# Kernel tuning notes

Measured on AMD Instinct MI355X. Metric: run time of the kernel, lower is better.

## Reference

```python
import jax, jax.numpy as jnp
import numpy as np
from jax.ops import segment_sum, segment_max, segment_min

B_, T_, V_, H_, W_ = 1, 8, 6, 96, 160
NUM_TRACKS = 512          # track ids in [-1, NUM_TRACKS)
THR = 2.0                 # distance_threshold
DKS = 0.05                # duplicate_keep_scale
NEG = -1e30


def setup_inputs() -> dict:
    key = jax.random.key(0)
    ks = jax.random.split(key, 10)
    shp = (B_, T_, V_, H_, W_)
    f = lambda k, c: jax.random.normal(k, shp + (c,), jnp.float32)
    return {
        "center": f(ks[0], 3),
        "offset": f(ks[1], 3),
        "opacity": f(ks[2], 1),
        "scale": f(ks[3], 3),
        "rotation": f(ks[4], 4),
        "feat_dc": f(ks[5], 3),
        "keep_score": f(ks[6], 1),
        "instance_affinity": f(ks[7], 32),
        "motion_code": f(ks[8], 16),
        "global_track_id": jax.random.randint(ks[9], shp, -1, NUM_TRACKS),
    }


def _merge(floats, gid):
    center, offset, opacity, scale, rotation, feat_dc, keep, inst, motion = floats
    b, t, v, h, w = gid.shape
    B, N = b * t, v * h * w
    BN = B * N
    S = B * NUM_TRACKS            # one segment per (frame, track id); S = dummy segment
    nseg = S + 1

    ids = gid.reshape(BN)
    bt = jnp.arange(BN) // N
    valid = ids >= 0
    seg = jnp.where(valid, bt * NUM_TRACKS + jnp.maximum(ids, 0), S)

    # tracks with >= 2 cells participate (torch: mask.sum() < 2 -> skip)
    cnt = segment_sum(valid.astype(jnp.int32), seg, num_segments=nseg)
    dup = valid & (cnt[seg] >= 2)
    seg1 = jnp.where(dup, seg, S)

    flat = lambda x: x.reshape(BN, x.shape[-1])
    k0 = flat(keep)[:, 0]
    c = flat(center)

    def seg_softmax(mask, sgm):
        # numerically stable segment softmax of k0 restricted to mask
        m = segment_max(jnp.where(mask, k0, NEG), sgm, num_segments=nseg)
        arg = jnp.where(mask, k0 - m[sgm], 0.0)   # keep grads finite on masked lanes
        e = jnp.where(mask, jnp.exp(arg), 0.0)
        z = segment_sum(e, sgm, num_segments=nseg)
        return e / jnp.maximum(z[sgm], 1e-20), m

    # pass 1: softmax-weighted mean center over all cells of the track
    w1, _ = seg_softmax(dup, seg1)
    mc1 = segment_sum(w1[:, None] * c, seg1, num_segments=nseg)
    dist = jnp.linalg.norm(c - mc1[seg1], axis=-1)
    active = dup & (dist <= THR)

    # pass 2: softmax restricted to active cells
    seg2 = jnp.where(active, seg, S)
    w2, m2 = seg_softmax(active, seg2)

    # representative = argmax weight (== argmax keep score), first occurrence on ties
    idx = jnp.arange(BN)
    cand = jnp.where(active & (k0 == m2[seg2]), idx, BN)
    rep = segment_min(cand, seg2, num_segments=nseg)
    is_rep = active & (idx == rep[seg2])

    def wmean(x):
        xf = flat(x)
        return segment_sum(w2[:, None] * xf, seg2, num_segments=nseg)[seg2]

    mcen = wmean(center)
    moff = wmean(offset)
    mop = wmean(opacity)
    msc = wmean(scale)
    mrot_seg = segment_sum(w2[:, None] * flat(rotation), seg2, num_segments=nseg)
    mrot_seg = mrot_seg / jnp.maximum(
        jnp.linalg.norm(mrot_seg, axis=-1, keepdims=True), 1e-12)  # F.normalize
    mrot = mrot_seg[seg2]
    mfd = wmean(feat_dc)
    minst = wmean(inst)
    mmot = wmean(motion)
    kf = flat(keep)
    mkeep = segment_max(jnp.where(active[:, None], kf, NEG), seg2,
                        num_segments=nseg)[seg2]

    a = active[:, None]
    sfac = jnp.where(is_rep, 1.0, DKS)[:, None]   # duplicates suppressed
    out = jnp.concatenate([
        jnp.where(a, mcen, c),
        jnp.where(a, moff, flat(offset)),
        jnp.where(a, mop * sfac, flat(opacity)),
        jnp.where(a, msc, flat(scale)),
        jnp.where(a, mrot, flat(rotation)),
        jnp.where(a, mfd, flat(feat_dc)),
        jnp.where(a, mkeep * sfac, kf),
        jnp.where(a, minst, flat(inst)),
        jnp.where(a, mmot, flat(motion)),
    ], axis=-1)
    return out.reshape(b, t, v, h, w, -1)


def reference(center, offset, opacity, scale, rotation, feat_dc, keep_score,
              instance_affinity, motion_code, global_track_id):
    floats = (center, offset, opacity, scale, rotation, feat_dc, keep_score,
              instance_affinity, motion_code)
    return _merge(floats, global_track_id)
```

## Files before the change

### kernel.cpp

```cpp
#include <hip/hip_runtime.h>

static constexpr int kBN   = 737280;
static constexpr int kSlab = 92160;
static constexpr int kNT   = 512;
static constexpr int kNSeg = 4096;
static constexpr int kChunk = 5120;

__global__ __launch_bounds__(1024) void k_count(const int* __restrict__ gid, int* cnt) {
    __shared__ int h[kNT];
    int tid = threadIdx.x;
    if (tid < kNT) h[tid] = 0;
    __syncthreads();
    int chunk0 = blockIdx.x * kChunk;
    int bt = chunk0 / kSlab;
    for (int j = tid; j < kChunk; j += 1024) {
        int id = gid[chunk0 + j];
        if (id >= 0) atomicAdd(&h[id], 1);
    }
    __syncthreads();
    if (tid < kNT) { int v = h[tid]; if (v) atomicAdd(&cnt[bt * kNT + tid], v); }
}

__global__ __launch_bounds__(1024) void k_scan(const int* __restrict__ cnt, int* offs, int* cursor) {
    __shared__ int part[1024];
    int tid = threadIdx.x;
    int b = tid * 4;
    int v0 = cnt[b], v1 = cnt[b + 1], v2 = cnt[b + 2], v3 = cnt[b + 3];
    int s01 = v0 + v1, s = s01 + v2 + v3;
    part[tid] = s;
    __syncthreads();
    for (int off = 1; off < 1024; off <<= 1) {
        int t = (tid >= off) ? part[tid - off] : 0;
        __syncthreads();
        part[tid] += t;
        __syncthreads();
    }
    int base = part[tid] - s;
    int o0 = base, o1 = base + v0, o2 = base + s01, o3 = base + s01 + v2;
    offs[b] = o0; offs[b + 1] = o1; offs[b + 2] = o2; offs[b + 3] = o3;
    cursor[b] = o0; cursor[b + 1] = o1; cursor[b + 2] = o2; cursor[b + 3] = o3;
}

__global__ __launch_bounds__(1024) void k_fill(const int* __restrict__ gid, int* cursor, int* lists) {
    __shared__ int lcnt[kNT];
    __shared__ int lbase[kNT];
    int tid = threadIdx.x;
    if (tid < kNT) lcnt[tid] = 0;
    __syncthreads();
    int chunk0 = blockIdx.x * kChunk;
    int bt = chunk0 / kSlab;
    int rank[5], ids[5];
#pragma unroll
    for (int u = 0; u < 5; u++) {
        int id = gid[chunk0 + tid + u * 1024];
        ids[u] = id;
        rank[u] = (id >= 0) ? atomicAdd(&lcnt[id], 1) : 0;
    }
    __syncthreads();
    if (tid < kNT) { int c = lcnt[tid]; lbase[tid] = c ? atomicAdd(&cursor[bt * kNT + tid], c) : 0; }
    __syncthreads();
#pragma unroll
    for (int u = 0; u < 5; u++) {
        int id = ids[u];
        if (id >= 0) lists[lbase[id] + rank[u]] = chunk0 + tid + u * 1024;
    }
}

template<int CNT>
__device__ __forceinline__ void wreduce_store(float (&a)[17], int lane, int tb, float* totl) {
#pragma unroll
    for (int c = 0; c < CNT; c++) {
        float v = a[c];
#pragma unroll
        for (int m = 1; m < 64; m <<= 1) v += __shfl_xor(v, m, 64);
        if (lane == 0) totl[tb + c] = v;
    }
}

__global__ __launch_bounds__(256, 4) void k_seg(
        const int* __restrict__ lists, const int* __restrict__ offs, const int* __restrict__ cnt,
        const float* __restrict__ keep, const float* __restrict__ center,
        const float* __restrict__ offsetp, const float* __restrict__ opacity,
        const float* __restrict__ scale, const float* __restrict__ rot,
        const float* __restrict__ fd, const float* __restrict__ inst,
        const float* __restrict__ motion,
        float* __restrict__ out) {
    int s = ((blockIdx.x & 7) << 9) | (blockIdx.x >> 3);
    int n = cnt[s];
    if (n < 2) return;
    int base = offs[s];
    int tid = threadIdx.x;
    int lane = tid & 63;
    int wv = tid >> 6;

    __shared__ int   idxs[256];
    __shared__ float kk[256];
    __shared__ float c0s[256], c1s[256], c2s[256];
    __shared__ float e2s[256];
    __shared__ float red4[256][5];
    __shared__ float wm1[4], wm2[4];
    __shared__ int   wri[4];
    __shared__ float totl[66];
    __shared__ float mrec[66];

    float lmax = -1e30f;
    for (int j = tid; j < n; j += 256) {
        int i = lists[base + j];
        float k = keep[i];
        float cx = center[3 * i + 0], cy = center[3 * i + 1], cz = center[3 * i + 2];
        if (j < 256) { idxs[j] = i; kk[j] = k; c0s[j] = cx; c1s[j] = cy; c2s[j] = cz; }
        lmax = fmaxf(lmax, k);
    }
#pragma unroll
    for (int m = 1; m < 64; m <<= 1) lmax = fmaxf(lmax, __shfl_xor(lmax, m, 64));
    if (lane == 0) wm1[wv] = lmax;
    __syncthreads();
    float m1 = fmaxf(fmaxf(wm1[0], wm1[1]), fmaxf(wm1[2], wm1[3]));

    float lz = 0.f, l0 = 0.f, l1 = 0.f, l2 = 0.f;
    for (int j = tid; j < n; j += 256) {
        float k, cx, cy, cz;
        if (j < 256) { k = kk[j]; cx = c0s[j]; cy = c1s[j]; cz = c2s[j]; }
        else { int i = lists[base + j]; k = keep[i];
               cx = center[3 * i + 0]; cy = center[3 * i + 1]; cz = center[3 * i + 2]; }
        float e = expf(k - m1);
        lz += e; l0 += e * cx; l1 += e * cy; l2 += e * cz;
    }
    red4[tid][0] = lz; red4[tid][1] = l0; red4[tid][2] = l1; red4[tid][3] = l2;
    __syncthreads();
    for (int o = 128; o; o >>= 1) {
        if (tid < o) {
            red4[tid][0] += red4[tid + o][0]; red4[tid][1] += red4[tid + o][1];
            red4[tid][2] += red4[tid + o][2]; red4[tid][3] += red4[tid + o][3];
        }
        __syncthreads();
    }
    float z1 = red4[0][0];
    float inv1 = 1.0f / fmaxf(z1, 1e-20f);
    float mc0 = red4[0][1] * inv1, mcy = red4[0][2] * inv1, mcz = red4[0][3] * inv1;

    float lm2 = -1e30f;
    for (int j = tid; j < n; j += 256) {
        float k, cx, cy, cz;
        if (j < 256) { k = kk[j]; cx = c0s[j]; cy = c1s[j]; cz = c2s[j]; }
        else { int i = lists[base + j]; k = keep[i];
               cx = center[3 * i + 0]; cy = center[3 * i + 1]; cz = center[3 * i + 2]; }
        float d0 = cx - mc0, d1 = cy - mcy, d2 = cz - mcz;
        bool act = sqrtf(d0 * d0 + d1 * d1 + d2 * d2) <= 2.0f;
        if (j < 256) e2s[j] = act ? 1.0f : 0.0f;
        if (act) lm2 = fmaxf(lm2, k);
    }
#pragma unroll
    for (int m = 1; m < 64; m <<= 1) lm2 = fmaxf(lm2, __shfl_xor(lm2, m, 64));
    if (lane == 0) wm2[wv] = lm2;
    __syncthreads();
    float m2 = fmaxf(fmaxf(wm2[0], wm2[1]), fmaxf(wm2[2], wm2[3]));

    int lrep = 0x7fffffff;
    for (int j = tid; j < n; j += 256) {
        if (j < 256) {
            bool act = e2s[j] != 0.0f;
            float k = kk[j];
            float e = act ? expf(k - m2) : 0.0f;
            e2s[j] = e;
            if (act && k == m2) lrep = min(lrep, idxs[j]);
        } else {
            int i = lists[base + j];
            float k = keep[i];
            float cx = center[3 * i + 0], cy = center[3 * i + 1], cz = center[3 * i + 2];
            float d0 = cx - mc0, d1 = cy - mcy, d2 = cz - mcz;
            if (sqrtf(d0 * d0 + d1 * d1 + d2 * d2) <= 2.0f && k == m2) lrep = min(lrep, i);
        }
    }
#pragma unroll
    for (int m = 1; m < 64; m <<= 1) lrep = min(lrep, __shfl_xor(lrep, m, 64));
    if (lane == 0) wri[wv] = lrep;
    __syncthreads();
    int rep = min(min(wri[0], wri[1]), min(wri[2], wri[3]));

    auto e2_glob = [&](int j, int& i) -> float {
        i = lists[base + j];
        float k = keep[i];
        float d0 = center[3 * i + 0] - mc0;
        float d1 = center[3 * i + 1] - mcy;
        float d2 = center[3 * i + 2] - mcz;
        return (sqrtf(d0 * d0 + d1 * d1 + d2 * d2) <= 2.0f) ? expf(k - m2) : 0.0f;
    };

    {
        float a[17];
#pragma unroll
        for (int c = 0; c < 17; c++) a[c] = 0.f;

        if (wv == 0) {
            for (int j = lane; j < n; j += 64) {
                float e, cx, cy, cz, k; int i;
                if (j < 256) { e = e2s[j]; i = idxs[j]; cx = c0s[j]; cy = c1s[j]; cz = c2s[j]; k = kk[j]; }
                else { e = e2_glob(j, i); k = keep[i];
                       cx = center[3 * i + 0]; cy = center[3 * i + 1]; cz = center[3 * i + 2]; }
                float o0 = offsetp[3 * i + 0], o1 = offsetp[3 * i + 1], o2 = offsetp[3 * i + 2];
                float op = opacity[i];
                float s0 = scale[3 * i + 0], s1 = scale[3 * i + 1], s2 = scale[3 * i + 2];
                float4 r4 = *(const float4*)(rot + 4 * i);
                float f0 = fd[3 * i + 0], f1 = fd[3 * i + 1], f2 = fd[3 * i + 2];
                if (e != 0.0f) {
                    a[0] += e * cx; a[1] += e * cy; a[2] += e * cz;
                    a[3] += e * o0; a[4] += e * o1; a[5] += e * o2;
                    a[6] += e * op;
                    a[7] += e * s0; a[8] += e * s1; a[9] += e * s2;
                    a[10] += e * r4.x; a[11] += e * r4.y; a[12] += e * r4.z; a[13] += e * r4.w;
                    a[14] += e * f0; a[15] += e * f1; a[16] += e * f2;
                } else {
                    float* o = out + (long)66 * i;
                    o[0] = cx; o[1] = cy; o[2] = cz;
                    o[3] = o0; o[4] = o1; o[5] = o2;
                    o[6] = op;
                    o[7] = s0; o[8] = s1; o[9] = s2;
                    o[10] = r4.x; o[11] = r4.y; o[12] = r4.z; o[13] = r4.w;
                    o[14] = f0; o[15] = f1; o[16] = f2;
                    o[17] = k;
                }
            }
            wreduce_store<17>(a, lane, 0, totl);
        } else if (wv == 1) {
            for (int j = lane; j < n; j += 64) {
                float e; int i;
                if (j < 256) { e = e2s[j]; i = idxs[j]; } else { e = e2_glob(j, i); }
                const float4* ip = (const float4*)(inst + 32 * i);
                float4 v0 = ip[0], v1 = ip[1], v2 = ip[2], v3 = ip[3];
                if (e != 0.0f) {
                    a[0]  += e * v0.x; a[1]  += e * v0.y; a[2]  += e * v0.z; a[3]  += e * v0.w;
                    a[4]  += e * v1.x; a[5]  += e * v1.y; a[6]  += e * v1.z; a[7]  += e * v1.w;
                    a[8]  += e * v2.x; a[9]  += e * v2.y; a[10] += e * v2.z; a[11] += e * v2.w;
                    a[12] += e * v3.x; a[13] += e * v3.y; a[14] += e * v3.z; a[15] += e * v3.w;
                } else {
                    float2* o = (float2*)(out + (long)66 * i + 18);
                    o[0] = make_float2(v0.x, v0.y); o[1] = make_float2(v0.z, v0.w);
                    o[2] = make_float2(v1.x, v1.y); o[3] = make_float2(v1.z, v1.w);
                    o[4] = make_float2(v2.x, v2.y); o[5] = make_float2(v2.z, v2.w);
                    o[6] = make_float2(v3.x, v3.y); o[7] = make_float2(v3.z, v3.w);
                }
            }
            wreduce_store<16>(a, lane, 17, totl);
        } else if (wv == 2) {
            for (int j = lane; j < n; j += 64) {
                float e; int i;
                if (j < 256) { e = e2s[j]; i = idxs[j]; } else { e = e2_glob(j, i); }
                const float4* ip = (const float4*)(inst + 32 * i) + 4;
                float4 v0 = ip[0], v1 = ip[1], v2 = ip[2], v3 = ip[3];
                if (e != 0.0f) {
                    a[0]  += e * v0.x; a[1]  += e * v0.y; a[2]  += e * v0.z; a[3]  += e * v0.w;
                    a[4]  += e * v1.x; a[5]  += e * v1.y; a[6]  += e * v1.z; a[7]  += e * v1.w;
                    a[8]  += e * v2.x; a[9]  += e * v2.y; a[10] += e * v2.z; a[11] += e * v2.w;
                    a[12] += e * v3.x; a[13] += e * v3.y; a[14] += e * v3.z; a[15] += e * v3.w;
                } else {
                    float2* o = (float2*)(out + (long)66 * i + 34);
                    o[0] = make_float2(v0.x, v0.y); o[1] = make_float2(v0.z, v0.w);
                    o[2] = make_float2(v1.x, v1.y); o[3] = make_float2(v1.z, v1.w);
                    o[4] = make_float2(v2.x, v2.y); o[5] = make_float2(v2.z, v2.w);
                    o[6] = make_float2(v3.x, v3.y); o[7] = make_float2(v3.z, v3.w);
                }
            }
            wreduce_store<16>(a, lane, 33, totl);
        } else {
            for (int j = lane; j < n; j += 64) {
                float e; int i;
                if (j < 256) { e = e2s[j]; i = idxs[j]; } else { e = e2_glob(j, i); }
                const float4* mp = (const float4*)(motion + 16 * i);
                float4 v0 = mp[0], v1 = mp[1], v2 = mp[2], v3 = mp[3];
                if (e != 0.0f) {
                    a[0]  += e * v0.x; a[1]  += e * v0.y; a[2]  += e * v0.z; a[3]  += e * v0.w;
                    a[4]  += e * v1.x; a[5]  += e * v1.y; a[6]  += e * v1.z; a[7]  += e * v1.w;
                    a[8]  += e * v2.x; a[9]  += e * v2.y; a[10] += e * v2.z; a[11] += e * v2.w;
                    a[12] += e * v3.x; a[13] += e * v3.y; a[14] += e * v3.z; a[15] += e * v3.w;
                    a[16] += e;
                } else {
                    float2* o = (float2*)(out + (long)66 * i + 50);
                    o[0] = make_float2(v0.x, v0.y); o[1] = make_float2(v0.z, v0.w);
                    o[2] = make_float2(v1.x, v1.y); o[3] = make_float2(v1.z, v1.w);
                    o[4] = make_float2(v2.x, v2.y); o[5] = make_float2(v2.z, v2.w);
                    o[6] = make_float2(v3.x, v3.y); o[7] = make_float2(v3.z, v3.w);
                }
            }
            wreduce_store<17>(a, lane, 49, totl);
        }
    }
    __syncthreads();

    if (tid < 66) {
        float z2v = totl[65];
        float inv2 = 1.0f / fmaxf(z2v, 1e-20f);
        float v;
        if (tid < 10) v = totl[tid] * inv2;
        else if (tid < 14) {
            float q0 = totl[10] * inv2, q1 = totl[11] * inv2;
            float q2 = totl[12] * inv2, q3 = totl[13] * inv2;
            float nrm = sqrtf(q0 * q0 + q1 * q1 + q2 * q2 + q3 * q3);
            float rn = 1.0f / fmaxf(nrm, 1e-12f);
            v = (totl[tid] * inv2) * rn;
        }
        else if (tid < 17) v = totl[tid] * inv2;
        else if (tid == 17) v = m2;
        else v = totl[tid - 1] * inv2;
        mrec[tid] = v;
    }
    __syncthreads();

    for (int f = tid; f < n * 33; f += 256) {
        int j = f / 33;
        int c2 = f - 33 * j;
        int i; bool act;
        if (j < 256) { act = e2s[j] != 0.0f; i = idxs[j]; }
        else { float e = e2_glob(j, i); act = e != 0.0f; }
        if (act) {
            float2 v = make_float2(mrec[2 * c2], mrec[2 * c2 + 1]);
            if (i != rep) {
                if (c2 == 3) v.x *= 0.05f;
                else if (c2 == 8) v.y *= 0.05f;
            }
            *(float2*)(out + (long)66 * i + 2 * c2) = v;
        }
    }
}

__global__ __launch_bounds__(256) void k_rest(
        const int* __restrict__ gid, const int* __restrict__ cnt,
        const float* __restrict__ keep, const float* __restrict__ center,
        const float* __restrict__ offsetp, const float* __restrict__ opacity,
        const float* __restrict__ scale, const float* __restrict__ rot,
        const float* __restrict__ fd, const float* __restrict__ inst,
        const float* __restrict__ motion,
        float* __restrict__ out) {
    int i = blockIdx.x * 256 + threadIdx.x;
    int id = gid[i];
    if (id >= 0 && cnt[(i / kSlab) * kNT + id] >= 2) return;
    float* o = out + (long)i * 66;
    o[0] = center[3 * i + 0]; o[1] = center[3 * i + 1]; o[2] = center[3 * i + 2];
#pragma unroll
    for (int c = 0; c < 3; c++) o[3 + c] = offsetp[3 * i + c];
    o[6] = opacity[i];
#pragma unroll
    for (int c = 0; c < 3; c++) o[7 + c] = scale[3 * i + c];
    float4 r4 = *(const float4*)(rot + 4 * i);
    o[10] = r4.x; o[11] = r4.y; o[12] = r4.z; o[13] = r4.w;
#pragma unroll
    for (int c = 0; c < 3; c++) o[14 + c] = fd[3 * i + c];
    o[17] = keep[i];
    const float4* ip = (const float4*)(inst + 32 * i);
#pragma unroll
    for (int q = 0; q < 8; q++) {
        float4 v = ip[q];
        o[18 + 4 * q + 0] = v.x; o[18 + 4 * q + 1] = v.y;
        o[18 + 4 * q + 2] = v.z; o[18 + 4 * q + 3] = v.w;
    }
    const float4* mp = (const float4*)(motion + 16 * i);
#pragma unroll
    for (int q = 0; q < 4; q++) {
        float4 v = mp[q];
        o[50 + 4 * q + 0] = v.x; o[50 + 4 * q + 1] = v.y;
        o[50 + 4 * q + 2] = v.z; o[50 + 4 * q + 3] = v.w;
    }
}

extern "C" void kernel_launch(void* const* d_in, const int* in_sizes, int n_in,
                              void* d_out, int out_size, void* d_ws, size_t ws_size,
                              hipStream_t stream) {
    const float* center = (const float*)d_in[0];
    const float* offsetp = (const float*)d_in[1];
    const float* opacity = (const float*)d_in[2];
    const float* scale = (const float*)d_in[3];
    const float* rot = (const float*)d_in[4];
    const float* fd = (const float*)d_in[5];
    const float* keep = (const float*)d_in[6];
    const float* inst = (const float*)d_in[7];
    const float* motion = (const float*)d_in[8];
    const int* gid = (const int*)d_in[9];
    float* out = (float*)d_out;

    int* cnt    = (int*)d_ws;
    int* offs   = (int*)d_ws + 4096;
    int* cursor = (int*)d_ws + 8192;
    int* lists  = (int*)d_ws + 12288;

    hipMemsetAsync(cnt, 0, (size_t)kNSeg * 4, stream);

    k_count<<<kBN / kChunk, 1024, 0, stream>>>(gid, cnt);
    k_scan<<<1, 1024, 0, stream>>>(cnt, offs, cursor);
    k_fill<<<kBN / kChunk, 1024, 0, stream>>>(gid, cursor, lists);
    k_seg<<<kNSeg, 256, 0, stream>>>(lists, offs, cnt, keep, center, offsetp, opacity,
                                     scale, rot, fd, inst, motion, out);
    k_rest<<<kBN / 256, 256, 0, stream>>>(gid, cnt, keep, center, offsetp, opacity, scale,
                                          rot, fd, inst, motion, out);
}
```

Baseline: 476.1 us.

## Map lanes to output channels in segment accumulation and writeback

Replaces the per-wave split by field group, where each lane handled one cell and all 17 fields, with a channel-major mapping. Each 16-lane group now handles one cell, and each lane covers up to 5 of the 66 channels through strided pointers. Accumulation becomes a two-step shuffle plus a shared-memory atomic instead of a full 64-lane reduction for every channel. The writeback loop drops the per-element division by 33, so each cell's row is written by adjacent lanes. This is meant to make output stores more contiguous and cut reduction cost, at the price of scalar strided input loads instead of float4 loads.

```diff
diff --git a/kernel.cpp b/kernel.cpp
--- a/kernel.cpp
+++ b/kernel.cpp
@@ -66,15 +66,19 @@
     }
 }
 
-template<int CNT>
-__device__ __forceinline__ void wreduce_store(float (&a)[17], int lane, int tb, float* totl) {
-#pragma unroll
-    for (int c = 0; c < CNT; c++) {
-        float v = a[c];
-#pragma unroll
-        for (int m = 1; m < 64; m <<= 1) v += __shfl_xor(v, m, 64);
-        if (lane == 0) totl[tb + c] = v;
-    }
+__device__ __forceinline__ const float* chan_ptr(int c,
+        const float* center, const float* offsetp, const float* opacity,
+        const float* scale, const float* rot, const float* fd,
+        const float* keep, const float* inst, const float* motion, int& stride) {
+    if (c < 3)  { stride = 3;  return center + c; }
+    if (c < 6)  { stride = 3;  return offsetp + (c - 3); }
+    if (c == 6) { stride = 1;  return opacity; }
+    if (c < 10) { stride = 3;  return scale + (c - 7); }
+    if (c < 14) { stride = 4;  return rot + (c - 10); }
+    if (c < 17) { stride = 3;  return fd + (c - 14); }
+    if (c == 17){ stride = 1;  return keep; }
+    if (c < 50) { stride = 32; return inst + (c - 18); }
+    stride = 16; return motion + (c - 50);
 }
 
 __global__ __launch_bounds__(256, 4) void k_seg(
@@ -175,121 +179,79 @@
 #pragma unroll
     for (int m = 1; m < 64; m <<= 1) lrep = min(lrep, __shfl_xor(lrep, m, 64));
     if (lane == 0) wri[wv] = lrep;
+    if (tid < 66) totl[tid] = 0.f;
     __syncthreads();
     int rep = min(min(wri[0], wri[1]), min(wri[2], wri[3]));
 
-    auto e2_glob = [&](int j, int& i) -> float {
-        i = lists[base + j];
-        float k = keep[i];
-        float d0 = center[3 * i + 0] - mc0;
-        float d1 = center[3 * i + 1] - mcy;
-        float d2 = center[3 * i + 2] - mcz;
-        return (sqrtf(d0 * d0 + d1 * d1 + d2 * d2) <= 2.0f) ? expf(k - m2) : 0.0f;
-    };
-
-    {
-        float a[17];
-#pragma unroll
-        for (int c = 0; c < 17; c++) a[c] = 0.f;
-
-        if (wv == 0) {
-            for (int j = lane; j < n; j += 64) {
-                float e, cx, cy, cz, k; int i;
-                if (j < 256) { e = e2s[j]; i = idxs[j]; cx = c0s[j]; cy = c1s[j]; cz = c2s[j]; k = kk[j]; }
-                else { e = e2_glob(j, i); k = keep[i];
-                       cx = center[3 * i + 0]; cy = center[3 * i + 1]; cz = center[3 * i + 2]; }
-                float o0 = offsetp[3 * i + 0], o1 = offsetp[3 * i + 1], o2 = offsetp[3 * i + 2];
-                float op = opacity[i];
-                float s0 = scale[3 * i + 0], s1 = scale[3 * i + 1], s2 = scale[3 * i + 2];
-                float4 r4 = *(const float4*)(rot + 4 * i);
-                float f0 = fd[3 * i + 0], f1 = fd[3 * i + 1], f2 = fd[3 * i + 2];
+    int g = lane >> 4;
+    int t = lane & 15;
+    const float* cptr[5]; int cstr[5]; int cch[5]; bool csf[5]; bool cok[5];
+#pragma unroll
+    for (int k = 0; k < 5; k++) {
+        int c = t + 16 * k;
+        cch[k] = c;
+        cok[k] = (c < 66);
+        if (c < 66) {
+            cptr[k] = chan_ptr(c, center, offsetp, opacity, scale, rot, fd, keep, inst, motion, cstr[k]);
+        } else { cptr[k] = opacity; cstr[k] = 0; }
+        csf[k] = (c == 6) || (c == 17);
+    }
+    float acc[5] = {0.f, 0.f, 0.f, 0.f, 0.f};
+    int jlim = n < 256 ? n : 256;
+
+    for (int jb = wv * 4 + g; jb < jlim; jb += 16) {
+        int i = idxs[jb];
+        float e = e2s[jb];
+        float v[5] = {0.f, 0.f, 0.f, 0.f, 0.f};
+#pragma unroll
+        for (int k = 0; k < 5; k++) if (cok[k]) v[k] = cptr[k][cstr[k] * i];
+        if (e != 0.0f) {
+#pragma unroll
+            for (int k = 0; k < 5; k++) if (cok[k])
+                acc[k] += e * ((cch[k] == 17) ? 1.0f : v[k]);
+        } else {
+            float* ob = out + 66 * (size_t)i;
+#pragma unroll
+            for (int k = 0; k < 5; k++) if (cok[k]) ob[t + 16 * k] = v[k];
+        }
+    }
+    if (n > 256) {
+        for (int j = 256 + wv; j < n; j += 4) {
+            int i = lists[base + j];
+            float kv = keep[i];
+            float cx = center[3 * i + 0], cy = center[3 * i + 1], cz = center[3 * i + 2];
+            float d0 = cx - mc0, d1 = cy - mcy, d2 = cz - mcz;
+            bool act = sqrtf(d0 * d0 + d1 * d1 + d2 * d2) <= 2.0f;
+            float e = act ? expf(kv - m2) : 0.0f;
+            if (g == 0) {
+                float v[5] = {0.f, 0.f, 0.f, 0.f, 0.f};
+#pragma unroll
+                for (int k = 0; k < 5; k++) if (cok[k]) v[k] = cptr[k][cstr[k] * i];
                 if (e != 0.0f) {
-                    a[0] += e * cx; a[1] += e * cy; a[2] += e * cz;
-                    a[3] += e * o0; a[4] += e * o1; a[5] += e * o2;
-                    a[6] += e * op;
-                    a[7] += e * s0; a[8] += e * s1; a[9] += e * s2;
-                    a[10] += e * r4.x; a[11] += e * r4.y; a[12] += e * r4.z; a[13] += e * r4.w;
-                    a[14] += e * f0; a[15] += e * f1; a[16] += e * f2;
+#pragma unroll
+                    for (int k = 0; k < 5; k++) if (cok[k])
+                        acc[k] += e * ((cch[k] == 17) ? 1.0f : v[k]);
                 } else {
-                    float* o = out + (long)66 * i;
-                    o[0] = cx; o[1] = cy; o[2] = cz;
-                    o[3] = o0; o[4] = o1; o[5] = o2;
-                    o[6] = op;
-                    o[7] = s0; o[8] = s1; o[9] = s2;
-                    o[10] = r4.x; o[11] = r4.y; o[12] = r4.z; o[13] = r4.w;
-                    o[14] = f0; o[15] = f1; o[16] = f2;
-                    o[17] = k;
+                    float* ob = out + 66 * (size_t)i;
+#pragma unroll
+                    for (int k = 0; k < 5; k++) if (cok[k]) ob[t + 16 * k] = v[k];
                 }
             }
-            wreduce_store<17>(a, lane, 0, totl);
-        } else if (wv == 1) {
-            for (int j = lane; j < n; j += 64) {
-                float e; int i;
-                if (j < 256) { e = e2s[j]; i = idxs[j]; } else { e = e2_glob(j, i); }
-                const float4* ip = (const float4*)(inst + 32 * i);
-                float4 v0 = ip[0], v1 = ip[1], v2 = ip[2], v3 = ip[3];
-                if (e != 0.0f) {
-                    a[0]  += e * v0.x; a[1]  += e * v0.y; a[2]  += e * v0.z; a[3]  += e * v0.w;
-                    a[4]  += e * v1.x; a[5]  += e * v1.y; a[6]  += e * v1.z; a[7]  += e * v1.w;
-                    a[8]  += e * v2.x; a[9]  += e * v2.y; a[10] += e * v2.z; a[11] += e * v2.w;
-                    a[12] += e * v3.x; a[13] += e * v3.y; a[14] += e * v3.z; a[15] += e * v3.w;
-                } else {
-                    float2* o = (float2*)(out + (long)66 * i + 18);
-                    o[0] = make_float2(v0.x, v0.y); o[1] = make_float2(v0.z, v0.w);
-                    o[2] = make_float2(v1.x, v1.y); o[3] = make_float2(v1.z, v1.w);
-                    o[4] = make_float2(v2.x, v2.y); o[5] = make_float2(v2.z, v2.w);
-                    o[6] = make_float2(v3.x, v3.y); o[7] = make_float2(v3.z, v3.w);
-                }
-            }
-            wreduce_store<16>(a, lane, 17, totl);
-        } else if (wv == 2) {
-            for (int j = lane; j < n; j += 64) {
-                float e; int i;
-                if (j < 256) { e = e2s[j]; i = idxs[j]; } else { e = e2_glob(j, i); }
-                const float4* ip = (const float4*)(inst + 32 * i) + 4;
-                float4 v0 = ip[0], v1 = ip[1], v2 = ip[2], v3 = ip[3];
-                if (e != 0.0f) {
-                    a[0]  += e * v0.x; a[1]  += e * v0.y; a[2]  += e * v0.z; a[3]  += e * v0.w;
-                    a[4]  += e * v1.x; a[5]  += e * v1.y; a[6]  += e * v1.z; a[7]  += e * v1.w;
-                    a[8]  += e * v2.x; a[9]  += e * v2.y; a[10] += e * v2.z; a[11] += e * v2.w;
-                    a[12] += e * v3.x; a[13] += e * v3.y; a[14] += e * v3.z; a[15] += e * v3.w;
-                } else {
-                    float2* o = (float2*)(out + (long)66 * i + 34);
-                    o[0] = make_float2(v0.x, v0.y); o[1] = make_float2(v0.z, v0.w);
-                    o[2] = make_float2(v1.x, v1.y); o[3] = make_float2(v1.z, v1.w);
-                    o[4] = make_float2(v2.x, v2.y); o[5] = make_float2(v2.z, v2.w);
-                    o[6] = make_float2(v3.x, v3.y); o[7] = make_float2(v3.z, v3.w);
-                }
-            }
-            wreduce_store<16>(a, lane, 33, totl);
-        } else {
-            for (int j = lane; j < n; j += 64) {
-                float e; int i;
-                if (j < 256) { e = e2s[j]; i = idxs[j]; } else { e = e2_glob(j, i); }
-                const float4* mp = (const float4*)(motion + 16 * i);
-                float4 v0 = mp[0], v1 = mp[1], v2 = mp[2], v3 = mp[3];
-                if (e != 0.0f) {
-                    a[0]  += e * v0.x; a[1]  += e * v0.y; a[2]  += e * v0.z; a[3]  += e * v0.w;
-                    a[4]  += e * v1.x; a[5]  += e * v1.y; a[6]  += e * v1.z; a[7]  += e * v1.w;
-                    a[8]  += e * v2.x; a[9]  += e * v2.y; a[10] += e * v2.z; a[11] += e * v2.w;
-                    a[12] += e * v3.x; a[13] += e * v3.y; a[14] += e * v3.z; a[15] += e * v3.w;
-                    a[16] += e;
-                } else {
-                    float2* o = (float2*)(out + (long)66 * i + 50);
-                    o[0] = make_float2(v0.x, v0.y); o[1] = make_float2(v0.z, v0.w);
-                    o[2] = make_float2(v1.x, v1.y); o[3] = make_float2(v1.z, v1.w);
-                    o[4] = make_float2(v2.x, v2.y); o[5] = make_float2(v2.z, v2.w);
-                    o[6] = make_float2(v3.x, v3.y); o[7] = make_float2(v3.z, v3.w);
-                }
-            }
-            wreduce_store<17>(a, lane, 49, totl);
-        }
+        }
+    }
+#pragma unroll
+    for (int k = 0; k < 5; k++) {
+        acc[k] += __shfl_xor(acc[k], 16, 64);
+        acc[k] += __shfl_xor(acc[k], 32, 64);
+    }
+    if (g == 0) {
+#pragma unroll
+        for (int k = 0; k < 5; k++) if (cok[k]) atomicAdd(&totl[cch[k]], acc[k]);
     }
     __syncthreads();
 
     if (tid < 66) {
-        float z2v = totl[65];
-        float inv2 = 1.0f / fmaxf(z2v, 1e-20f);
+        float inv2 = 1.0f / fmaxf(totl[17], 1e-20f);
         float v;
         if (tid < 10) v = totl[tid] * inv2;
         else if (tid < 14) {
@@ -301,24 +263,46 @@
         }
         else if (tid < 17) v = totl[tid] * inv2;
         else if (tid == 17) v = m2;
-        else v = totl[tid - 1] * inv2;
+        else v = totl[tid] * inv2;
         mrec[tid] = v;
     }
     __syncthreads();
 
-    for (int f = tid; f < n * 33; f += 256) {
-        int j = f / 33;
-        int c2 = f - 33 * j;
-        int i; bool act;
-        if (j < 256) { act = e2s[j] != 0.0f; i = idxs[j]; }
-        else { float e = e2_glob(j, i); act = e != 0.0f; }
-        if (act) {
-            float2 v = make_float2(mrec[2 * c2], mrec[2 * c2 + 1]);
-            if (i != rep) {
-                if (c2 == 3) v.x *= 0.05f;
-                else if (c2 == 8) v.y *= 0.05f;
+    float mv[5];
+#pragma unroll
+    for (int k = 0; k < 5; k++) mv[k] = cok[k] ? mrec[cch[k]] : 0.f;
+    for (int jb = wv * 4 + g; jb < jlim; jb += 16) {
+        float e = e2s[jb];
+        if (e != 0.0f) {
+            int i = idxs[jb];
+            bool ns = (i != rep);
+            float* ob = out + 66 * (size_t)i;
+#pragma unroll
+            for (int k = 0; k < 5; k++) if (cok[k]) {
+                float v = mv[k];
+                if (csf[k] && ns) v *= 0.05f;
+                ob[t + 16 * k] = v;
             }
-            *(float2*)(out + (long)66 * i + 2 * c2) = v;
+        }
+    }
+    if (n > 256) {
+        for (int j = 256 + wv; j < n; j += 4) {
+            int i = lists[base + j];
+            float kv = keep[i];
+            float cx = center[3 * i + 0], cy = center[3 * i + 1], cz = center[3 * i + 2];
+            float d0 = cx - mc0, d1 = cy - mcy, d2 = cz - mcz;
+            bool act = sqrtf(d0 * d0 + d1 * d1 + d2 * d2) <= 2.0f;
+            (void)kv;
+            if (act && g == 0) {
+                bool ns = (i != rep);
+                float* ob = out + 66 * (size_t)i;
+#pragma unroll
+                for (int k = 0; k < 5; k++) if (cok[k]) {
+                    float v = mv[k];
+                    if (csf[k] && ns) v *= 0.05f;
+                    ob[t + 16 * k] = v;
+                }
+            }
         }
     }
 }
```

Measured after the change: 502.0 us. +5.4%, slower.
